# Performance work log

Measured on AMD Instinct MI355X. Metric: run time of the kernel, lower is better.

## Reference

```python
import jax, jax.numpy as jnp
import numpy as np

PI = float(np.pi)
DT = 0.05
N_STEPS = 5
DIFF_SCALE = 0.3


def wrap_to_pi(t):
    return (t + PI) % (2.0 * PI) - PI


def setup_inputs() -> dict:
    key = jax.random.key(0)
    ks = jax.random.split(key, 24)
    B, T, d, H, C = 1024, 256, 256, 128, 64
    s = 0.05  # generic init scale for weights
    inp = {
        "context_angles": jax.random.normal(ks[0], (B, T, d), dtype=jnp.float32),
        # Brownian increments over n_steps fixed solver steps: dW ~ N(0, dt)
        "dW": jax.random.normal(ks[1], (B, N_STEPS, d), dtype=jnp.float32) * np.sqrt(DT).astype(np.float32),
        # equinox GRUCell params: weight_ih (3H, 2d), weight_hh (3H, H), bias (3H), bias_n (H)
        "gru_wih": jax.random.normal(ks[2], (3 * H, 2 * d)) * s,
        "gru_whh": jax.random.normal(ks[3], (3 * H, H)) * s,
        "gru_b": jax.random.normal(ks[4], (3 * H,)) * s,
        "gru_bn": jax.random.normal(ks[5], (H,)) * s,
        "proj_w": jax.random.normal(ks[6], (C, H)) * s,
        "proj_b": jax.random.normal(ks[7], (C,)) * s,
        # drift MLP (depth=3): 576 -> 128 -> 128 -> 128 -> 256, last bias zeroed
        "dr_w0": jax.random.normal(ks[8], (H, 2 * d + C)) * s,
        "dr_b0": jax.random.normal(ks[9], (H,)) * s,
        "dr_w1": jax.random.normal(ks[10], (H, H)) * s,
        "dr_b1": jax.random.normal(ks[11], (H,)) * s,
        "dr_w2": jax.random.normal(ks[12], (H, H)) * s,
        "dr_b2": jax.random.normal(ks[13], (H,)) * s,
        "dr_w3": jax.random.normal(ks[14], (d, H)) * s,
        "dr_b3": jnp.zeros((d,), dtype=jnp.float32),
        # diffusion MLP (depth=2): 576 -> 128 -> 128 -> 256, last weight *0.1, bias = -2.0
        "df_w0": jax.random.normal(ks[15], (H, 2 * d + C)) * s,
        "df_b0": jax.random.normal(ks[16], (H,)) * s,
        "df_w1": jax.random.normal(ks[17], (H, H)) * s,
        "df_b1": jax.random.normal(ks[18], (H,)) * s,
        "df_w2": jax.random.normal(ks[19], (d, H)) * s * 0.1,
        "df_b2": jnp.full((d,), -2.0, dtype=jnp.float32),
    }
    return inp


def reference(context_angles, dW, gru_wih, gru_whh, gru_b, gru_bn,
              proj_w, proj_b,
              dr_w0, dr_b0, dr_w1, dr_b1, dr_w2, dr_b2, dr_w3, dr_b3,
              df_w0, df_b0, df_w1, df_b1, df_w2, df_b2):
    B, T, d = context_angles.shape
    H = gru_whh.shape[1]

    # sin/cos angle features: (B, T, 2d), scanned over time (batched GRU)
    feats = jnp.concatenate([jnp.sin(context_angles), jnp.cos(context_angles)], axis=-1)
    x_seq = jnp.swapaxes(feats, 0, 1)  # (T, B, 2d)

    def gru_step(h, x):
        gi = x @ gru_wih.T + gru_b        # (B, 3H)
        gh = h @ gru_whh.T                # (B, 3H)
        ir, iz, in_ = jnp.split(gi, 3, axis=-1)
        hr, hz, hn = jnp.split(gh, 3, axis=-1)
        r = jax.nn.sigmoid(ir + hr)
        z = jax.nn.sigmoid(iz + hz)
        n = jnp.tanh(in_ + r * (hn + gru_bn))
        h_new = n + z * (h - n)
        return h_new, None

    h0 = jnp.zeros((B, H), dtype=feats.dtype)
    h_final, _ = jax.lax.scan(gru_step, h0, x_seq)
    ctx = h_final @ proj_w.T + proj_b  # (B, ctx_dim)

    silu = jax.nn.silu

    def drift(inp):  # (B, 2d+C) -> (B, d); coeffs in identity frame of flat torus
        h = silu(inp @ dr_w0.T + dr_b0)
        h = silu(h @ dr_w1.T + dr_b1)
        h = silu(h @ dr_w2.T + dr_b2)
        return h @ dr_w3.T + dr_b3

    def diffusion_scales(inp):  # diagonal diffusion: frame = identity on flat torus
        h = silu(inp @ df_w0.T + df_b0)
        h = silu(h @ df_w1.T + df_b1)
        return jax.nn.softplus(h @ df_w2.T + df_b2) * DIFF_SCALE

    # geometric SDE integration: exp-map on flat torus = wrap(theta + v)
    theta = wrap_to_pi(context_angles[:, -1])  # (B, d)
    for k in range(N_STEPS):
        inp = jnp.concatenate([jnp.sin(theta), jnp.cos(theta), ctx], axis=-1)
        mu = drift(inp)
        sg = diffusion_scales(inp)
        theta = wrap_to_pi(theta + mu * DT + sg * dW[:, k])
    return theta
```

## Files before the change

### kernel.cpp

```cpp
#include <hip/hip_runtime.h>
#include <stdint.h>

#define PI_F      3.14159265358979323846f
#define TWO_PI_F  6.28318530717958647692f
#define DT_F      0.05f
#define DIFF_SCALE_F 0.3f

typedef short short8 __attribute__((ext_vector_type(8)));
typedef float f32x4 __attribute__((ext_vector_type(4)));
typedef float f32x2 __attribute__((ext_vector_type(2)));
typedef unsigned int u32x4 __attribute__((ext_vector_type(4)));
typedef unsigned int u32x2 __attribute__((ext_vector_type(2)));

__device__ __forceinline__ unsigned short f2bf(float x) {
    unsigned int u = __float_as_uint(x);
    u += 0x7FFFu + ((u >> 16) & 1u);
    return (unsigned short)(u >> 16);
}
__device__ __forceinline__ float bf2f(unsigned short h) {
    return __uint_as_float(((unsigned int)h) << 16);
}
__device__ __forceinline__ unsigned int cvtpk_bf16(float lo, float hi) {
    unsigned int r;
    asm("v_cvt_pk_bf16_f32 %0, %1, %2" : "=v"(r) : "v"(lo), "v"(hi));
    return r;
}
__device__ __forceinline__ float siluf(float x) {
    return x / (1.0f + __expf(-x));
}
__device__ __forceinline__ float wrapf(float t) {
    float w = fmodf(t + PI_F, TWO_PI_F);
    w = (w < 0.0f) ? w + TWO_PI_F : w;
    return w - PI_F;
}
__device__ __forceinline__ float dot4(const float* __restrict__ W, const float* __restrict__ X, int K) {
    float a = 0.0f;
#pragma unroll 4
    for (int kk = 0; kk < K; kk += 4) {
        f32x4 wv = *(const f32x4*)(W + kk);
        f32x4 xv = *(const f32x4*)(X + kk);
        a += wv[0]*xv[0] + wv[1]*xv[1] + wv[2]*xv[2] + wv[3]*xv[3];
    }
    return a;
}

#define SYNC_RAW() do { \
    asm volatile("s_waitcnt lgkmcnt(0)" ::: "memory"); \
    __builtin_amdgcn_s_barrier(); \
    __builtin_amdgcn_sched_barrier(0); \
} while (0)

__global__ void prep_kernel(const float* __restrict__ wih, const float* __restrict__ whh,
                            unsigned short* __restrict__ wihp, unsigned short* __restrict__ whhb) {
    int i = blockIdx.x * 256 + threadIdx.x;
    if (i < 196608) {
        int e = i & 7, lane = (i >> 3) & 63, rest = i >> 9;
        int ns = rest % 6, ki = (rest / 6) & 1, half = (rest / 12) & 1;
        int dt = (rest / 24) & 3, w = rest / 96;
        int col = w*96 + ns*16 + (lane & 15);
        int k   = half*256 + dt*64 + ki*32 + (lane >> 4)*8 + e;
        wihp[i] = f2bf(wih[col*512 + k]);
    }
    if (i < 384*128) whhb[i] = f2bf(whh[i]);
}

__global__ void prep2_kernel(const float* __restrict__ dr_w0, const float* __restrict__ dr_w1,
                             const float* __restrict__ dr_w2, const float* __restrict__ dr_w3,
                             const float* __restrict__ df_w0, const float* __restrict__ df_w1,
                             const float* __restrict__ df_w2,
                             unsigned short* __restrict__ dst) {
    int i = blockIdx.x * 256 + threadIdx.x;
    int e = i & 7, lane = (i >> 3) & 63;
    int l15 = lane & 15, l4 = lane >> 4;
    const float* src; int base, K, wide;
    if      (i < 73728)  { src = dr_w0; base = 0;      K = 576; wide = 0; }
    else if (i < 90112)  { src = dr_w1; base = 73728;  K = 128; wide = 0; }
    else if (i < 106496) { src = dr_w2; base = 90112;  K = 128; wide = 0; }
    else if (i < 139264) { src = dr_w3; base = 106496; K = 128; wide = 1; }
    else if (i < 212992) { src = df_w0; base = 139264; K = 576; wide = 0; }
    else if (i < 229376) { src = df_w1; base = 212992; K = 128; wide = 0; }
    else                 { src = df_w2; base = 229376; K = 128; wide = 1; }
    int lr = (i - base) >> 9;
    int nks = (K == 576) ? 18 : 4;
    int j, k;
    if (!wide) {
        int w = lr / nks, ks = lr % nks;
        j = w*16 + l15;
        k = ks*32 + l4*8 + e;
    } else {
        int ks = lr & 3, tile = (lr >> 2) & 1, w = lr >> 3;
        j = w*32 + tile*16 + l15;
        k = ks*32 + l4*8 + e;
    }
    dst[i] = f2bf(src[(size_t)j*K + k]);
}

__launch_bounds__(256, 4)
__global__ void gi_gemm_kernel(const float* __restrict__ ctx_ang,
                               const unsigned short* __restrict__ wihp,
                               unsigned int* __restrict__ P01,
                               unsigned short* __restrict__ P2) {
    __shared__ __align__(16) float ctxL[4][32*64];
    __shared__ __align__(16) unsigned short As[2][32*64];

    const int tid  = threadIdx.x;
    const int lane = tid & 63;
    const int w    = tid >> 6;
    const int l15  = lane & 15;
    const int l4   = lane >> 4;
    const int mt   = blockIdx.x;
    const int t    = mt >> 5;
    const int b0   = (mt & 31) * 32;

    const int l4r = lane >> 4;
    const int c4  = (lane & 15) * 4;

    f32x4 acc[2][6];
    const f32x4 z4 = {0.0f, 0.0f, 0.0f, 0.0f};
#pragma unroll
    for (int mi = 0; mi < 2; ++mi)
#pragma unroll
        for (int ns = 0; ns < 6; ++ns) acc[mi][ns] = z4;

#pragma unroll
    for (int dt = 0; dt < 4; ++dt) {
#pragma unroll
        for (int i = 0; i < 2; ++i) {
            const float* src = ctx_ang + ((size_t)(b0 + w*8 + i*4 + l4r) * 65536
                                          + (size_t)t * 256 + dt*64 + c4);
            void* dst = (void*)((char*)&ctxL[dt][0] + (w*8 + i*4) * 256);
            __builtin_amdgcn_global_load_lds(
                (const __attribute__((address_space(1))) unsigned int*)src,
                (__attribute__((address_space(3))) unsigned int*)dst, 16, 0, 0);
        }
    }
    asm volatile("s_waitcnt vmcnt(0)" ::: "memory");
    __builtin_amdgcn_s_barrier();
    __builtin_amdgcn_sched_barrier(0);

#pragma unroll
    for (int dt = 0; dt < 4; ++dt) {
        {
            f32x4 cv[2];
#pragma unroll
            for (int r = 0; r < 2; ++r)
                cv[r] = *(const f32x4*)((const char*)&ctxL[dt][0] + tid*16 + r*4096);
#pragma unroll
            for (int r = 0; r < 2; ++r) {
                int row = (tid >> 4) + r*16;
                int c0  = (tid & 15) * 4;
                unsigned int s01 = cvtpk_bf16(__sinf(cv[r][0]), __sinf(cv[r][1]));
                unsigned int s23 = cvtpk_bf16(__sinf(cv[r][2]), __sinf(cv[r][3]));
                unsigned int c01 = cvtpk_bf16(__cosf(cv[r][0]), __cosf(cv[r][1]));
                unsigned int c23 = cvtpk_bf16(__cosf(cv[r][2]), __cosf(cv[r][3]));
                int boff = row*128 + (((c0 >> 3) ^ (row & 7)) * 16) + (c0 & 7) * 2;
                u32x2 sv = { s01, s23 };
                u32x2 cc = { c01, c23 };
                *(u32x2*)((char*)&As[0][0] + boff) = sv;
                *(u32x2*)((char*)&As[1][0] + boff) = cc;
            }
        }
        SYNC_RAW();

#pragma unroll
        for (int half = 0; half < 2; ++half) {
            const char* Ab = (const char*)&As[half][0];
#pragma unroll
            for (int ki = 0; ki < 2; ++ki) {
                short8 aF[2], bF[6];
#pragma unroll
                for (int mi = 0; mi < 2; ++mi) {
                    int row = mi*16 + l15;
                    int kg  = ki*4 + l4;
                    aF[mi] = *(const short8*)(Ab + row*128 + ((kg ^ (row & 7)))*16);
                }
#pragma unroll
                for (int ns = 0; ns < 6; ++ns) {
                    int fidx = (((w*4 + dt)*2 + half)*2 + ki)*6 + ns;
                    bF[ns] = *(const short8*)(wihp + ((size_t)fidx*64 + lane)*8);
                }
#pragma unroll
                for (int mi = 0; mi < 2; ++mi)
#pragma unroll
                    for (int ns = 0; ns < 6; ++ns)
                        acc[mi][ns] = __builtin_amdgcn_mfma_f32_16x16x32_bf16(aF[mi], bF[ns], acc[mi][ns], 0, 0, 0);
            }
        }
        SYNC_RAW();
    }

    {
        char* stg = (char*)&ctxL[0][0];
#pragma unroll
        for (int mi = 0; mi < 2; ++mi) {
#pragma unroll
            for (int ns = 0; ns < 6; ++ns) {
                int col = w*96 + ns*16 + l15;
                int g = col >> 7, j = col & 127;
#pragma unroll
                for (int r = 0; r < 4; ++r) {
                    int b = mi*16 + l4*4 + r;
                    unsigned short vv = f2bf(acc[mi][ns][r]);
                    if (g < 2) *(unsigned short*)(stg + ((size_t)(b*128 + j))*4 + g*2) = vv;
                    else       *(unsigned short*)(stg + 16384 + ((size_t)(b*128 + j))*2) = vv;
                }
            }
        }
        SYNC_RAW();
        const u32x4* s01v = (const u32x4*)stg;
        u32x4* dst01 = (u32x4*)(P01 + ((size_t)t*1024 + b0)*128);
#pragma unroll
        for (int e = 0; e < 4; ++e)
            dst01[tid + e*256] = s01v[tid + e*256];
        const u32x4* s2v = (const u32x4*)(stg + 16384);
        u32x4* dst2 = (u32x4*)(P2 + ((size_t)t*1024 + b0)*128);
#pragma unroll
        for (int e = 0; e < 2; ++e)
            dst2[tid + e*256] = s2v[tid + e*256];
    }
}


#define LOADPF(PA, PB, tt) do { \
    if ((tt) < 256) { \
        size_t _i = ((size_t)(tt)*1024 + b0 + l4)*128 + j; \
        PA = P01[_i]; \
        PB = P2[_i]; \
    } \
} while (0)

#define STEP(RDBUF, WRBUF, PA, PB, TT) do { \
    short8 aF[4]; \
    _Pragma("unroll") \
    for (int kt = 0; kt < 4; ++kt) \
        aF[kt] = *(const short8*)((const char*)(RDBUF) + l15*256 + (((kt*4 + l4) ^ (l15 & 7)))*16); \
    f32x4 q0[4], q1[4], q2[4]; \
    _Pragma("unroll") \
    for (int kt = 0; kt < 4; ++kt) { \
        q0[kt] = __builtin_amdgcn_mfma_f32_16x16x32_bf16(aF[kt], whB0[kt], z4, 0, 0, 0); \
        q1[kt] = __builtin_amdgcn_mfma_f32_16x16x32_bf16(aF[kt], whB1[kt], z4, 0, 0, 0); \
        q2[kt] = __builtin_amdgcn_mfma_f32_16x16x32_bf16(aF[kt], whB2[kt], z4, 0, 0, 0); \
    } \
    float g0 = (q0[0][0] + q0[1][0]) + (q0[2][0] + q0[3][0]); \
    float g1 = (q1[0][0] + q1[1][0]) + (q1[2][0] + q1[3][0]); \
    float g2 = (q2[0][0] + q2[1][0]) + (q2[2][0] + q2[3][0]); \
    unsigned int _pa = PA; unsigned short _pb = PB; \
    LOADPF(PA, PB, TT); \
    { \
        float ir  = bf2f((unsigned short)(_pa & 0xFFFFu)) + bR; \
        float iz  = bf2f((unsigned short)(_pa >> 16))     + bZ; \
        float in_ = bf2f(_pb)                             + bN; \
        float rg = __builtin_amdgcn_rcpf(1.0f + __expf(-(ir + g0))); \
        float zg = __builtin_amdgcn_rcpf(1.0f + __expf(-(iz + g1))); \
        float ng = 1.0f - 2.0f*__builtin_amdgcn_rcpf(1.0f + __expf(2.0f*(in_ + rg*(g2 + bBN)))); \
        H = ng + zg*(H - ng); \
        int row = l4*4; \
        *(unsigned short*)((char*)(WRBUF) + row*256 + (((j >> 3) ^ (row & 7))*16) + (j & 7)*2) = f2bf(H); \
    } \
    SYNC_RAW(); \
} while (0)

__launch_bounds__(512, 4)
__global__ void scan_kernel(const unsigned int* __restrict__ P01,
                            const unsigned short* __restrict__ P2,
                            const unsigned short* __restrict__ whhb,
                            const float* __restrict__ gru_b,
                            const float* __restrict__ gru_bn,
                            float* __restrict__ h_ws) {
    __shared__ __align__(16) unsigned short hAbuf[2][16*128];

    const int tid  = threadIdx.x;
    const int lane = tid & 63;
    const int w    = tid >> 6;
    const int l15  = lane & 15;
    const int l4   = lane >> 4;
    const int b0   = blockIdx.x * 4;
    const int j    = w*16 + l15;

    {
        u32x4 z = {0u,0u,0u,0u};
        *(u32x4*)((char*)hAbuf + tid*16) = z;
    }

    short8 whB0[4], whB1[4], whB2[4];
#pragma unroll
    for (int kt = 0; kt < 4; ++kt) {
        whB0[kt] = *(const short8*)(whhb + (size_t)(0*128 + j)*128 + kt*32 + l4*8);
        whB1[kt] = *(const short8*)(whhb + (size_t)(1*128 + j)*128 + kt*32 + l4*8);
        whB2[kt] = *(const short8*)(whhb + (size_t)(2*128 + j)*128 + kt*32 + l4*8);
    }
    const float bR  = gru_b[j];
    const float bZ  = gru_b[128 + j];
    const float bN  = gru_b[256 + j];
    const float bBN = gru_bn[j];

    float H = 0.f;
    const f32x4 z4 = {0.0f,0.0f,0.0f,0.0f};

    unsigned int  PAa = 0, PAb = 0, PAc = 0, PAd = 0;
    unsigned short PBa = 0, PBb = 0, PBc = 0, PBd = 0;
    LOADPF(PAa, PBa, 0);
    LOADPF(PAb, PBb, 1);
    LOADPF(PAc, PBc, 2);
    LOADPF(PAd, PBd, 3);
    __syncthreads();

    for (int t = 0; t < 256; t += 4) {
        STEP(&hAbuf[0][0], &hAbuf[1][0], PAa, PBa, t + 4);
        STEP(&hAbuf[1][0], &hAbuf[0][0], PAb, PBb, t + 5);
        STEP(&hAbuf[0][0], &hAbuf[1][0], PAc, PBc, t + 6);
        STEP(&hAbuf[1][0], &hAbuf[0][0], PAd, PBd, t + 7);
    }

    h_ws[(size_t)(b0 + l4)*128 + j] = H;
}

#define AFRAG(BUF, S, ks) (*(const short8*)((const char*)(BUF) + l15*(S) + ((((ks)*4 + l4) ^ (l15 & 7))*16)))
#define PF18(W, ks) (*(const short8*)((W) + (((size_t)(w*18 + (ks)))*64 + lane)*8))
#define PF4(W, ks)  (*(const short8*)((W) + (((size_t)(w*4 + (ks)))*64 + lane)*8))
#define PFW(W, tile, ks) (*(const short8*)((W) + (((size_t)((w*2 + (tile))*4 + (ks)))*64 + lane)*8))
#define HSTORE(BUF, bb, col, val) (*(unsigned short*)((char*)(BUF) + (bb)*256 + ((((col)>>3) ^ ((bb)&7))*16) + ((col)&7)*2) = f2bf(val))
#define MFMA16(af, bf, c) __builtin_amdgcn_mfma_f32_16x16x32_bf16((af), (bf), (c), 0, 0, 0)

__launch_bounds__(512, 1)
__global__ void sde_kernel(const float* __restrict__ ctx_ang,
                           const float* __restrict__ dW,
                           const float* __restrict__ proj_w,
                           const float* __restrict__ proj_b,
                           const float* __restrict__ dr_b0, const float* __restrict__ dr_b1,
                           const float* __restrict__ dr_b2, const float* __restrict__ dr_b3,
                           const float* __restrict__ df_b0, const float* __restrict__ df_b1,
                           const float* __restrict__ df_b2,
                           const unsigned short* __restrict__ W0d, const unsigned short* __restrict__ W1d,
                           const unsigned short* __restrict__ W2d, const unsigned short* __restrict__ W3d,
                           const unsigned short* __restrict__ W0f, const unsigned short* __restrict__ W1f,
                           const unsigned short* __restrict__ W2f,
                           const float* __restrict__ h_ws,
                           float* __restrict__ out) {
    __shared__ __align__(16) float th[4*256];
    __shared__ __align__(16) float ctxs[4*64];
    __shared__ __align__(16) float h32[4*128];
    __shared__ __align__(16) unsigned short inpA[16*576];
    __shared__ __align__(16) unsigned short hA[16*128], hB[16*128], hC[16*128], hD[16*128];

    const int tid  = threadIdx.x;
    const int lane = tid & 63;
    const int w    = tid >> 6;
    const int l15  = lane & 15;
    const int l4   = lane >> 4;
    const int b0   = blockIdx.x * 4;
    const f32x4 z4 = {0.f,0.f,0.f,0.f};

    h32[tid & 511] = 0.0f;
    __syncthreads();
    ((float*)h32)[tid] = h_ws[(size_t)b0*128 + tid];
    __syncthreads();
    if (tid < 256) {
        int b = tid >> 6, c = tid & 63;
        ctxs[tid] = proj_b[c] + dot4(proj_w + (size_t)c*128, h32 + b*128, 128);
    }
#pragma unroll
    for (int e = 0; e < 2; ++e) {
        int idx = tid + e*512; int b = idx >> 8, i = idx & 255;
        th[idx] = wrapf(ctx_ang[((size_t)(b0 + b)*256 + 255)*256 + i]);
    }

    const int j  = w*16 + l15;
    const int j20 = w*32 + l15;
    const int j21 = w*32 + 16 + l15;
    const float bd0 = dr_b0[j], bd1 = dr_b1[j], bd2 = dr_b2[j];
    const float bf0 = df_b0[j], bf1 = df_b1[j];
    const float bd3t0 = dr_b3[j20], bd3t1 = dr_b3[j21];
    const float bf2t0 = df_b2[j20], bf2t1 = df_b2[j21];
    __syncthreads();

    for (int k = 0; k < 5; ++k) {
#pragma unroll
        for (int e = 0; e < 5; ++e) {
            int idx = tid + e*512;
            if (idx < 2304) {
                int b = idx / 576;
                int i = idx - b*576;
                float vv;
                if (i < 256)      vv = __sinf(th[(b<<8) + i]);
                else if (i < 512) vv = __cosf(th[(b<<8) + i - 256]);
                else              vv = ctxs[(b<<6) + i - 512];
                *(unsigned short*)((char*)inpA + b*1152 + (((i>>3) ^ (b&7))*16) + (i&7)*2) = f2bf(vv);
            }
        }
        __syncthreads();

        {
            f32x4 a0=z4,a1=z4,c0=z4,c1=z4;
#pragma unroll
            for (int ks = 0; ks < 18; ks += 2) {
                short8 af0 = AFRAG(inpA, 1152, ks);
                short8 af1 = AFRAG(inpA, 1152, ks+1);
                a0 = MFMA16(af0, PF18(W0d, ks),   a0);
                c0 = MFMA16(af0, PF18(W0f, ks),   c0);
                a1 = MFMA16(af1, PF18(W0d, ks+1), a1);
                c1 = MFMA16(af1, PF18(W0f, ks+1), c1);
            }
#pragma unroll
            for (int r = 0; r < 4; ++r) {
                int bb = l4*4 + r;
                HSTORE(hA, bb, j, siluf(a0[r] + a1[r] + bd0));
                HSTORE(hC, bb, j, siluf(c0[r] + c1[r] + bf0));
            }
        }
        __syncthreads();

        {
            f32x4 a0=z4,a1=z4,c0=z4,c1=z4;
#pragma unroll
            for (int ks = 0; ks < 4; ks += 2) {
                short8 aA0 = AFRAG(hA, 256, ks), aA1 = AFRAG(hA, 256, ks+1);
                short8 aC0 = AFRAG(hC, 256, ks), aC1 = AFRAG(hC, 256, ks+1);
                a0 = MFMA16(aA0, PF4(W1d, ks),   a0);
                c0 = MFMA16(aC0, PF4(W1f, ks),   c0);
                a1 = MFMA16(aA1, PF4(W1d, ks+1), a1);
                c1 = MFMA16(aC1, PF4(W1f, ks+1), c1);
            }
#pragma unroll
            for (int r = 0; r < 4; ++r) {
                int bb = l4*4 + r;
                HSTORE(hB, bb, j, siluf(a0[r] + a1[r] + bd1));
                HSTORE(hD, bb, j, siluf(c0[r] + c1[r] + bf1));
            }
        }
        __syncthreads();

        float sgr[2][4];
        {
            f32x4 a0=z4,a1=z4,s0=z4,s1=z4,s2=z4,s3=z4;
#pragma unroll
            for (int ks = 0; ks < 4; ks += 2) {
                short8 b0f = AFRAG(hB, 256, ks), b1f = AFRAG(hB, 256, ks+1);
                short8 d0f = AFRAG(hD, 256, ks), d1f = AFRAG(hD, 256, ks+1);
                a0 = MFMA16(b0f, PF4(W2d, ks),   a0);
                a1 = MFMA16(b1f, PF4(W2d, ks+1), a1);
                s0 = MFMA16(d0f, PFW(W2f, 0, ks),   s0);
                s1 = MFMA16(d1f, PFW(W2f, 0, ks+1), s1);
                s2 = MFMA16(d0f, PFW(W2f, 1, ks),   s2);
                s3 = MFMA16(d1f, PFW(W2f, 1, ks+1), s3);
            }
#pragma unroll
            for (int r = 0; r < 4; ++r) {
                int bb = l4*4 + r;
                HSTORE(hA, bb, j, siluf(a0[r] + a1[r] + bd2));
                float aa0 = s0[r] + s1[r] + bf2t0;
                float aa1 = s2[r] + s3[r] + bf2t1;
                float sp0 = (aa0 > 15.f) ? aa0 : log1pf(__expf(aa0));
                float sp1 = (aa1 > 15.f) ? aa1 : log1pf(__expf(aa1));
                sgr[0][r] = sp0 * DIFF_SCALE_F;
                sgr[1][r] = sp1 * DIFF_SCALE_F;
            }
        }
        __syncthreads();

        {
            f32x4 m0=z4,m1=z4,m2=z4,m3=z4;
#pragma unroll
            for (int ks = 0; ks < 4; ks += 2) {
                short8 h0f = AFRAG(hA, 256, ks), h1f = AFRAG(hA, 256, ks+1);
                m0 = MFMA16(h0f, PFW(W3d, 0, ks),   m0);
                m1 = MFMA16(h1f, PFW(W3d, 0, ks+1), m1);
                m2 = MFMA16(h0f, PFW(W3d, 1, ks),   m2);
                m3 = MFMA16(h1f, PFW(W3d, 1, ks+1), m3);
            }
            if (l4 == 0) {
#pragma unroll
                for (int r = 0; r < 4; ++r) {
                    int bb = r;
                    {
                        float mu = m0[r] + m1[r] + bd3t0;
                        float dw = dW[((size_t)(b0 + bb)*5 + k)*256 + j20];
                        th[(bb<<8) + j20] = wrapf(th[(bb<<8) + j20] + mu*DT_F + sgr[0][r]*dw);
                    }
                    {
                        float mu = m2[r] + m3[r] + bd3t1;
                        float dw = dW[((size_t)(b0 + bb)*5 + k)*256 + j21];
                        th[(bb<<8) + j21] = wrapf(th[(bb<<8) + j21] + mu*DT_F + sgr[1][r]*dw);
                    }
                }
            }
        }
        __syncthreads();
    }

#pragma unroll
    for (int e = 0; e < 2; ++e) {
        int idx = tid + e*512;
        out[(size_t)b0*256 + idx] = th[idx];
    }
}

extern "C" void kernel_launch(void* const* d_in, const int* in_sizes, int n_in,
                              void* d_out, int out_size, void* d_ws, size_t ws_size,
                              hipStream_t stream) {
    const float* ctx_ang = (const float*)d_in[0];
    const float* dW      = (const float*)d_in[1];
    const float* wih     = (const float*)d_in[2];
    const float* whh     = (const float*)d_in[3];
    const float* gru_b   = (const float*)d_in[4];
    const float* gru_bn  = (const float*)d_in[5];
    const float* proj_w  = (const float*)d_in[6];
    const float* proj_b  = (const float*)d_in[7];
    const float* dr_w0   = (const float*)d_in[8];
    const float* dr_b0   = (const float*)d_in[9];
    const float* dr_w1   = (const float*)d_in[10];
    const float* dr_b1   = (const float*)d_in[11];
    const float* dr_w2   = (const float*)d_in[12];
    const float* dr_b2   = (const float*)d_in[13];
    const float* dr_w3   = (const float*)d_in[14];
    const float* dr_b3   = (const float*)d_in[15];
    const float* df_w0   = (const float*)d_in[16];
    const float* df_b0   = (const float*)d_in[17];
    const float* df_w1   = (const float*)d_in[18];
    const float* df_b1   = (const float*)d_in[19];
    const float* df_w2   = (const float*)d_in[20];
    const float* df_b2   = (const float*)d_in[21];
    float* out = (float*)d_out;

    char* ws = (char*)d_ws;
    unsigned int*   P01  = (unsigned int*)ws;
    unsigned short* P2   = (unsigned short*)(ws + 134217728);
    unsigned short* wihp = (unsigned short*)(ws + 201326592);
    unsigned short* whhb = (unsigned short*)(ws + 201719808);
    float*          h_ws = (float*)(ws + 201818112);

    unsigned short* Wb  = (unsigned short*)ws;
    unsigned short* W0d = Wb;
    unsigned short* W1d = Wb + 73728;
    unsigned short* W2d = Wb + 90112;
    unsigned short* W3d = Wb + 106496;
    unsigned short* W0f = Wb + 139264;
    unsigned short* W1f = Wb + 212992;
    unsigned short* W2f = Wb + 229376;

    prep_kernel<<<768, 256, 0, stream>>>(wih, whh, wihp, whhb);
    gi_gemm_kernel<<<8192, 256, 0, stream>>>(ctx_ang, wihp, P01, P2);
    scan_kernel<<<256, 512, 0, stream>>>(P01, P2, whhb, gru_b, gru_bn, h_ws);
    prep2_kernel<<<1024, 256, 0, stream>>>(dr_w0, dr_w1, dr_w2, dr_w3, df_w0, df_w1, df_w2, Wb);
    sde_kernel<<<256, 512, 0, stream>>>(ctx_ang, dW,
        proj_w, proj_b, dr_b0, dr_b1, dr_b2, dr_b3, df_b0, df_b1, df_b2,
        W0d, W1d, W2d, W3d, W0f, W1f, W2f, h_ws, out);
}
```

Baseline: 399.2 us.

## Warp-specialize GI GEMM into producer and MFMA consumer waves with double buffering

The input-projection GEMM kernel now runs 512 threads: four producer waves load context angles directly into registers, compute sin/cos and write bf16 tiles into a double-buffered LDS region. Four consumer waves run the MFMA over the previous tile, so trig computation and global loads overlap with matrix math. The old bulk global-to-LDS prefetch with its full wait is gone. In exchange, every block holds twice as many threads, and half the waves sit idle during either phase.

```diff
diff --git a/kernel.cpp b/kernel.cpp
--- a/kernel.cpp
+++ b/kernel.cpp
@@ -95,25 +95,29 @@
     dst[i] = f2bf(src[(size_t)j*K + k]);
 }
 
-__launch_bounds__(256, 4)
+__launch_bounds__(512, 2)
 __global__ void gi_gemm_kernel(const float* __restrict__ ctx_ang,
                                const unsigned short* __restrict__ wihp,
                                unsigned int* __restrict__ P01,
                                unsigned short* __restrict__ P2) {
-    __shared__ __align__(16) float ctxL[4][32*64];
-    __shared__ __align__(16) unsigned short As[2][32*64];
+    __shared__ __align__(16) unsigned short As[2][2][32*64];
+    __shared__ __align__(16) char stg[24576];
 
     const int tid  = threadIdx.x;
     const int lane = tid & 63;
-    const int w    = tid >> 6;
+    const int wv   = tid >> 6;
+    const bool isProd = (wv < 4);
     const int l15  = lane & 15;
     const int l4   = lane >> 4;
     const int mt   = blockIdx.x;
     const int t    = mt >> 5;
     const int b0   = (mt & 31) * 32;
 
-    const int l4r = lane >> 4;
-    const int c4  = (lane & 15) * 4;
+    const int prow = tid >> 3;
+    const int pseg = tid & 7;
+    const float* psrc0 = ctx_ang + ((size_t)(b0 + prow) * 65536 + (size_t)t * 256 + pseg * 8);
+
+    const int w2 = wv - 4;
 
     f32x4 acc[2][6];
     const f32x4 z4 = {0.0f, 0.0f, 0.0f, 0.0f};
@@ -122,102 +126,101 @@
 #pragma unroll
         for (int ns = 0; ns < 6; ++ns) acc[mi][ns] = z4;
 
-#pragma unroll
-    for (int dt = 0; dt < 4; ++dt) {
-#pragma unroll
-        for (int i = 0; i < 2; ++i) {
-            const float* src = ctx_ang + ((size_t)(b0 + w*8 + i*4 + l4r) * 65536
-                                          + (size_t)t * 256 + dt*64 + c4);
-            void* dst = (void*)((char*)&ctxL[dt][0] + (w*8 + i*4) * 256);
-            __builtin_amdgcn_global_load_lds(
-                (const __attribute__((address_space(1))) unsigned int*)src,
-                (__attribute__((address_space(3))) unsigned int*)dst, 16, 0, 0);
-        }
-    }
-    asm volatile("s_waitcnt vmcnt(0)" ::: "memory");
-    __builtin_amdgcn_s_barrier();
-    __builtin_amdgcn_sched_barrier(0);
-
-#pragma unroll
-    for (int dt = 0; dt < 4; ++dt) {
-        {
-            f32x4 cv[2];
-#pragma unroll
-            for (int r = 0; r < 2; ++r)
-                cv[r] = *(const f32x4*)((const char*)&ctxL[dt][0] + tid*16 + r*4096);
-#pragma unroll
-            for (int r = 0; r < 2; ++r) {
-                int row = (tid >> 4) + r*16;
-                int c0  = (tid & 15) * 4;
-                unsigned int s01 = cvtpk_bf16(__sinf(cv[r][0]), __sinf(cv[r][1]));
-                unsigned int s23 = cvtpk_bf16(__sinf(cv[r][2]), __sinf(cv[r][3]));
-                unsigned int c01 = cvtpk_bf16(__cosf(cv[r][0]), __cosf(cv[r][1]));
-                unsigned int c23 = cvtpk_bf16(__cosf(cv[r][2]), __cosf(cv[r][3]));
-                int boff = row*128 + (((c0 >> 3) ^ (row & 7)) * 16) + (c0 & 7) * 2;
-                u32x2 sv = { s01, s23 };
-                u32x2 cc = { c01, c23 };
-                *(u32x2*)((char*)&As[0][0] + boff) = sv;
-                *(u32x2*)((char*)&As[1][0] + boff) = cc;
-            }
+    f32x4 ra[2], rb[2];
+#define PLOAD(slot, dt_) do { \
+    ra[slot] = *(const f32x4*)(psrc0 + (dt_)*64); \
+    rb[slot] = *(const f32x4*)(psrc0 + (dt_)*64 + 4); \
+} while (0)
+
+#define PPROC(slot, buf_) do { \
+    f32x4 _a = ra[slot], _b = rb[slot]; \
+    unsigned int s0 = cvtpk_bf16(__sinf(_a[0]), __sinf(_a[1])); \
+    unsigned int s1 = cvtpk_bf16(__sinf(_a[2]), __sinf(_a[3])); \
+    unsigned int s2 = cvtpk_bf16(__sinf(_b[0]), __sinf(_b[1])); \
+    unsigned int s3 = cvtpk_bf16(__sinf(_b[2]), __sinf(_b[3])); \
+    unsigned int c0 = cvtpk_bf16(__cosf(_a[0]), __cosf(_a[1])); \
+    unsigned int c1 = cvtpk_bf16(__cosf(_a[2]), __cosf(_a[3])); \
+    unsigned int c2 = cvtpk_bf16(__cosf(_b[0]), __cosf(_b[1])); \
+    unsigned int c3 = cvtpk_bf16(__cosf(_b[2]), __cosf(_b[3])); \
+    int boff = prow*128 + ((pseg ^ (prow & 7)) * 16); \
+    u32x4 sv = { s0, s1, s2, s3 }; \
+    u32x4 cc = { c0, c1, c2, c3 }; \
+    *(u32x4*)((char*)&As[buf_][0][0] + boff) = sv; \
+    *(u32x4*)((char*)&As[buf_][1][0] + boff) = cc; \
+} while (0)
+
+#define CMFMA(dt_, buf_) do { \
+    _Pragma("unroll") \
+    for (int half = 0; half < 2; ++half) { \
+        const char* Ab = (const char*)&As[buf_][half][0]; \
+        _Pragma("unroll") \
+        for (int ki = 0; ki < 2; ++ki) { \
+            short8 aF[2], bF[6]; \
+            _Pragma("unroll") \
+            for (int mi = 0; mi < 2; ++mi) { \
+                int row = mi*16 + l15; \
+                int kg  = ki*4 + l4; \
+                aF[mi] = *(const short8*)(Ab + row*128 + ((kg ^ (row & 7)))*16); \
+            } \
+            _Pragma("unroll") \
+            for (int ns = 0; ns < 6; ++ns) { \
+                int fidx = (((w2*4 + (dt_))*2 + half)*2 + ki)*6 + ns; \
+                bF[ns] = *(const short8*)(wihp + ((size_t)fidx*64 + lane)*8); \
+            } \
+            _Pragma("unroll") \
+            for (int mi = 0; mi < 2; ++mi) \
+                _Pragma("unroll") \
+                for (int ns = 0; ns < 6; ++ns) \
+                    acc[mi][ns] = __builtin_amdgcn_mfma_f32_16x16x32_bf16(aF[mi], bF[ns], acc[mi][ns], 0, 0, 0); \
+        } \
+    } \
+} while (0)
+
+    if (isProd) PLOAD(0, 0);
+
+#pragma unroll
+    for (int p = 0; p < 5; ++p) {
+        if (p < 4 && isProd) {
+            if (p < 3) PLOAD((p + 1) & 1, p + 1);
+            PPROC(p & 1, p & 1);
+        }
+        if (p >= 1 && !isProd) {
+            CMFMA(p - 1, (p - 1) & 1);
         }
         SYNC_RAW();
-
-#pragma unroll
-        for (int half = 0; half < 2; ++half) {
-            const char* Ab = (const char*)&As[half][0];
-#pragma unroll
-            for (int ki = 0; ki < 2; ++ki) {
-                short8 aF[2], bF[6];
-#pragma unroll
-                for (int mi = 0; mi < 2; ++mi) {
-                    int row = mi*16 + l15;
-                    int kg  = ki*4 + l4;
-                    aF[mi] = *(const short8*)(Ab + row*128 + ((kg ^ (row & 7)))*16);
-                }
-#pragma unroll
-                for (int ns = 0; ns < 6; ++ns) {
-                    int fidx = (((w*4 + dt)*2 + half)*2 + ki)*6 + ns;
-                    bF[ns] = *(const short8*)(wihp + ((size_t)fidx*64 + lane)*8);
-                }
-#pragma unroll
-                for (int mi = 0; mi < 2; ++mi)
-#pragma unroll
-                    for (int ns = 0; ns < 6; ++ns)
-                        acc[mi][ns] = __builtin_amdgcn_mfma_f32_16x16x32_bf16(aF[mi], bF[ns], acc[mi][ns], 0, 0, 0);
-            }
-        }
-        SYNC_RAW();
-    }
-
-    {
-        char* stg = (char*)&ctxL[0][0];
+    }
+
+    if (!isProd) {
 #pragma unroll
         for (int mi = 0; mi < 2; ++mi) {
 #pragma unroll
             for (int ns = 0; ns < 6; ++ns) {
-                int col = w*96 + ns*16 + l15;
+                int col = w2*96 + ns*16 + l15;
                 int g = col >> 7, j = col & 127;
 #pragma unroll
                 for (int r = 0; r < 4; ++r) {
                     int b = mi*16 + l4*4 + r;
-                    unsigned short vv = f2bf(acc[mi][ns][r]);
-                    if (g < 2) *(unsigned short*)(stg + ((size_t)(b*128 + j))*4 + g*2) = vv;
-                    else       *(unsigned short*)(stg + 16384 + ((size_t)(b*128 + j))*2) = vv;
+                    unsigned short vvv = f2bf(acc[mi][ns][r]);
+                    if (g < 2) *(unsigned short*)(stg + ((size_t)(b*128 + j))*4 + g*2) = vvv;
+                    else       *(unsigned short*)(stg + 16384 + ((size_t)(b*128 + j))*2) = vvv;
                 }
             }
         }
-        SYNC_RAW();
+    }
+    SYNC_RAW();
+    {
         const u32x4* s01v = (const u32x4*)stg;
         u32x4* dst01 = (u32x4*)(P01 + ((size_t)t*1024 + b0)*128);
 #pragma unroll
-        for (int e = 0; e < 4; ++e)
-            dst01[tid + e*256] = s01v[tid + e*256];
+        for (int e = 0; e < 2; ++e)
+            dst01[tid + e*512] = s01v[tid + e*512];
         const u32x4* s2v = (const u32x4*)(stg + 16384);
         u32x4* dst2 = (u32x4*)(P2 + ((size_t)t*1024 + b0)*128);
-#pragma unroll
-        for (int e = 0; e < 2; ++e)
-            dst2[tid + e*256] = s2v[tid + e*256];
-    }
+        dst2[tid] = s2v[tid];
+    }
+#undef PLOAD
+#undef PPROC
+#undef CMFMA
 }
 
 
@@ -539,7 +542,7 @@
     unsigned short* W2f = Wb + 229376;
 
     prep_kernel<<<768, 256, 0, stream>>>(wih, whh, wihp, whhb);
-    gi_gemm_kernel<<<8192, 256, 0, stream>>>(ctx_ang, wihp, P01, P2);
+    gi_gemm_kernel<<<8192, 512, 0, stream>>>(ctx_ang, wihp, P01, P2);
     scan_kernel<<<256, 512, 0, stream>>>(P01, P2, whhb, gru_b, gru_bn, h_ws);
     prep2_kernel<<<1024, 256, 0, stream>>>(dr_w0, dr_w1, dr_w2, dr_w3, df_w0, df_w1, df_w2, Wb);
     sde_kernel<<<256, 512, 0, stream>>>(ctx_ang, dW,
```

Measured after the change: 450.3 us. +12.8%, slower.
